# Kernel tuning notes

Hardware: AMD Instinct MI355X
Metric: run time of the kernel (lower is better)

Reference implementation:

```python
import jax, jax.numpy as jnp
import numpy as np

S, B, D, H, E, HID = 512, 16, 768, 12, 8, 3072
HD = D // H
EPS = 1e-5


def _ln(x, w, b):
    m = jnp.mean(x, axis=-1, keepdims=True)
    v = jnp.var(x, axis=-1, keepdims=True)
    return (x - m) * jax.lax.rsqrt(v + EPS) * w + b


def setup_inputs() -> dict:
    key = jax.random.key(0)
    ks = jax.random.split(key, 9)
    n = lambda k, *sh: jax.random.normal(k, sh, dtype=jnp.float32) * 0.02
    return dict(
        x=jax.random.normal(ks[0], (S, B, D), dtype=jnp.float32),
        ln1_w=jnp.ones((D,), jnp.float32), ln1_b=jnp.zeros((D,), jnp.float32),
        wq=n(ks[1], D, D), bq=jnp.zeros((D,), jnp.float32),
        wk=n(ks[2], D, D), bk=jnp.zeros((D,), jnp.float32),
        wv=n(ks[3], D, D), bv=jnp.zeros((D,), jnp.float32),
        wo=n(ks[4], D, D), bo=jnp.zeros((D,), jnp.float32),
        ln2_w=jnp.ones((D,), jnp.float32), ln2_b=jnp.zeros((D,), jnp.float32),
        wg=n(ks[5], D, E), bg=jnp.zeros((E,), jnp.float32),
        w1=n(ks[6], E, D, HID), b1=jnp.zeros((E, HID), jnp.float32),
        w2=n(ks[7], E, HID, D), b2=jnp.zeros((E, D), jnp.float32),
    )


def _block(x, ln1_w, ln1_b, wq, bq, wk, bk, wv, bv, wo, bo,
           ln2_w, ln2_b, wg, bg, w1, b1, w2, b2):
    # --- attention: source uses query = norm1(x), key = value = x ---
    q_in = _ln(x, ln1_w, ln1_b)
    q = (q_in @ wq + bq).reshape(S, B, H, HD)
    k = (x @ wk + bk).reshape(S, B, H, HD)
    v = (x @ wv + bv).reshape(S, B, H, HD)
    scores = jnp.einsum('sbhd,tbhd->bhst', q, k) * (1.0 / HD ** 0.5)
    p = jax.nn.softmax(scores, axis=-1)
    attn = jnp.einsum('bhst,tbhd->sbhd', p, v).reshape(S, B, D)
    x = x + attn @ wo + bo
    # --- top-1 MoE MLP on norm2(x) ---
    t = _ln(x, ln2_w, ln2_b).reshape(S * B, D)   # [T, D] routed tokens
    logits = t @ wg + bg                          # [T, E]
    probs = jax.nn.softmax(logits, axis=-1)
    idx = jnp.argmax(logits, axis=-1)             # top-1 expert per token
    gate = jnp.take_along_axis(probs, idx[:, None], axis=-1)   # [T, 1]
    comb = jax.nn.one_hot(idx, E, dtype=t.dtype) * gate        # [T, E]

    def expert(w1e, b1e, w2e, b2e):
        return jax.nn.gelu(t @ w1e + b1e, approximate=False) @ w2e + b2e

    y = jax.vmap(expert)(w1, b1, w2, b2)          # [E, T, D]
    moe = jnp.einsum('te,etd->td', comb, y).reshape(S, B, D)
    return x + moe


def reference(x, ln1_w, ln1_b, wq, bq, wk, bk, wv, bv, wo, bo,
              ln2_w, ln2_b, wg, bg, w1, b1, w2, b2):
    return _block(x, ln1_w, ln1_b, wq, bq, wk, bk, wv, bv, wo, bo,
                  ln2_w, ln2_b, wg, bg, w1, b1, w2, b2)
```

## Files before the change

kernel.cpp:

```cpp
#include <hip/hip_runtime.h>
#include <math.h>

#define SS 512
#define BB 16
#define DD 768
#define HH 12
#define HDIM 64
#define EE 8
#define HID 3072
#define TT 8192
#define EPSV 1e-5f
#define KVSTR 1536
#define ASTR 72
#define NBANK 64

typedef __attribute__((ext_vector_type(8))) short s16x8;
typedef __attribute__((ext_vector_type(4))) short s16x4;
typedef __attribute__((ext_vector_type(4))) float f32x4;

__device__ inline short f2bf(float f) {
  unsigned u = __builtin_bit_cast(unsigned, f);
  unsigned r = (u + 0x7fffu + ((u >> 16) & 1u)) >> 16;
  return (short)r;
}

__device__ inline float gelu_f(float x) {
  float y = 0.7978845608028654f * (x + 0.044715f * x * x * x);
  float e = __expf(2.f * y);
  float t = 1.f - 2.f / (e + 1.f);
  return 0.5f * x * (1.f + t);
}

__device__ inline void gl2lds16(const void* g, void* l) {
  __builtin_amdgcn_global_load_lds(
      (const __attribute__((address_space(1))) unsigned int*)g,
      (__attribute__((address_space(3))) unsigned int*)l, 16, 0, 0);
}

__global__ __launch_bounds__(256) void transpose4_bf16(const float* __restrict__ w0,
    const float* __restrict__ w1p, const float* __restrict__ w2p,
    const float* __restrict__ w3p, short* __restrict__ dst) {
  const int z = blockIdx.z;
  const float* W = (z == 0) ? w0 : (z == 1) ? w1p : (z == 2) ? w2p : w3p;
  short* Wt = dst + (size_t)z * DD * DD;
  int k0 = blockIdx.x * 64, n0 = blockIdx.y * 64;
  __shared__ float t[64][65];
  for (int i = threadIdx.x; i < 1024; i += 256) {
    int r = i >> 4, c4 = (i & 15) << 2;
    const float4 v = *(const float4*)(W + (size_t)(k0 + r) * DD + n0 + c4);
    t[r][c4] = v.x; t[r][c4 + 1] = v.y; t[r][c4 + 2] = v.z; t[r][c4 + 3] = v.w;
  }
  __syncthreads();
  for (int i = threadIdx.x; i < 1024; i += 256) {
    int r = i >> 4, c4 = (i & 15) << 2;
    s16x4 sv;
    sv.x = f2bf(t[c4][r]);     sv.y = f2bf(t[c4 + 1][r]);
    sv.z = f2bf(t[c4 + 2][r]); sv.w = f2bf(t[c4 + 3][r]);
    *(s16x4*)(Wt + (size_t)(n0 + r) * DD + k0 + c4) = sv;
  }
}

__global__ __launch_bounds__(256) void transpose_bf16(const float* __restrict__ W,
    short* __restrict__ Wt, int K, int N) {
  const float* Wz = W + (size_t)blockIdx.z * K * N;
  short* Wtz = Wt + (size_t)blockIdx.z * K * N;
  int k0 = blockIdx.x * 64, n0 = blockIdx.y * 64;
  __shared__ float t[64][65];
  for (int i = threadIdx.x; i < 1024; i += 256) {
    int r = i >> 4, c4 = (i & 15) << 2;
    const float4 v = *(const float4*)(Wz + (size_t)(k0 + r) * N + n0 + c4);
    t[r][c4] = v.x; t[r][c4 + 1] = v.y; t[r][c4 + 2] = v.z; t[r][c4 + 3] = v.w;
  }
  __syncthreads();
  for (int i = threadIdx.x; i < 1024; i += 256) {
    int r = i >> 4, c4 = (i & 15) << 2;
    s16x4 sv;
    sv.x = f2bf(t[c4][r]);     sv.y = f2bf(t[c4 + 1][r]);
    sv.z = f2bf(t[c4 + 2][r]); sv.w = f2bf(t[c4 + 3][r]);
    *(s16x4*)(Wtz + (size_t)(n0 + r) * K + k0 + c4) = sv;
  }
}

__global__ __launch_bounds__(256) void gate_transpose(const float* __restrict__ wg,
    float* __restrict__ wgT) {
  for (int i = threadIdx.x + blockIdx.x * 256; i < EE * DD; i += 256 * 8) {
    int e = i / DD, d = i - e * DD;
    wgT[i] = wg[d * EE + e];
  }
}

__global__ __launch_bounds__(256) void fused_cvt_ln1(const float* __restrict__ x,
    const float* __restrict__ w, const float* __restrict__ b,
    short* __restrict__ xbf, short* __restrict__ ln1bf) {
  const int tok = blockIdx.x * 4 + (threadIdx.x >> 6);
  const int lane = threadIdx.x & 63;
  const float* row = x + (size_t)tok * DD;
  const float4 v0 = *(const float4*)(row + lane * 4);
  const float4 v1 = *(const float4*)(row + 256 + lane * 4);
  const float4 v2 = *(const float4*)(row + 512 + lane * 4);
  float s = v0.x + v0.y + v0.z + v0.w + v1.x + v1.y + v1.z + v1.w
          + v2.x + v2.y + v2.z + v2.w;
  float ss = v0.x * v0.x + v0.y * v0.y + v0.z * v0.z + v0.w * v0.w
           + v1.x * v1.x + v1.y * v1.y + v1.z * v1.z + v1.w * v1.w
           + v2.x * v2.x + v2.y * v2.y + v2.z * v2.z + v2.w * v2.w;
#pragma unroll
  for (int o = 1; o < 64; o <<= 1) { s += __shfl_xor(s, o); ss += __shfl_xor(ss, o); }
  const float mean = s * (1.f / DD);
  const float inv = rsqrtf(ss * (1.f / DD) - mean * mean + EPSV);
  short* xrow = xbf + (size_t)tok * DD;
  short* lrow = ln1bf + (size_t)tok * DD;
#define LN1_CHUNK(v, off) { \
  const float4 wv = *(const float4*)(w + (off) + lane * 4); \
  const float4 bv = *(const float4*)(b + (off) + lane * 4); \
  s16x4 xa, la; \
  xa.x = f2bf(v.x); xa.y = f2bf(v.y); xa.z = f2bf(v.z); xa.w = f2bf(v.w); \
  la.x = f2bf((v.x - mean) * inv * wv.x + bv.x); \
  la.y = f2bf((v.y - mean) * inv * wv.y + bv.y); \
  la.z = f2bf((v.z - mean) * inv * wv.z + bv.z); \
  la.w = f2bf((v.w - mean) * inv * wv.w + bv.w); \
  *(s16x4*)(xrow + (off) + lane * 4) = xa; \
  *(s16x4*)(lrow + (off) + lane * 4) = la; }
  LN1_CHUNK(v0, 0)
  LN1_CHUNK(v1, 256)
  LN1_CHUNK(v2, 512)
#undef LN1_CHUNK
}

__global__ __launch_bounds__(256) void fused_ln2_route(const float* __restrict__ x1,
    const float* __restrict__ w, const float* __restrict__ b,
    const float* __restrict__ wgT, const float* __restrict__ bg,
    short* __restrict__ tlnbf, int* __restrict__ idx, float* __restrict__ gate,
    int* __restrict__ cnt2) {
  const int tok = blockIdx.x * 4 + (threadIdx.x >> 6);
  const int lane = threadIdx.x & 63;
  const float* row = x1 + (size_t)tok * DD;
  const float4 v0 = *(const float4*)(row + lane * 4);
  const float4 v1 = *(const float4*)(row + 256 + lane * 4);
  const float4 v2 = *(const float4*)(row + 512 + lane * 4);
  float s = v0.x + v0.y + v0.z + v0.w + v1.x + v1.y + v1.z + v1.w
          + v2.x + v2.y + v2.z + v2.w;
  float ss = v0.x * v0.x + v0.y * v0.y + v0.z * v0.z + v0.w * v0.w
           + v1.x * v1.x + v1.y * v1.y + v1.z * v1.z + v1.w * v1.w
           + v2.x * v2.x + v2.y * v2.y + v2.z * v2.z + v2.w * v2.w;
#pragma unroll
  for (int o = 1; o < 64; o <<= 1) { s += __shfl_xor(s, o); ss += __shfl_xor(ss, o); }
  const float mean = s * (1.f / DD);
  const float inv = rsqrtf(ss * (1.f / DD) - mean * mean + EPSV);
  short* srow = tlnbf + (size_t)tok * DD;
  float acc[EE];
#pragma unroll
  for (int e = 0; e < EE; ++e) acc[e] = 0.f;
#define LN2_CHUNK(v, off) { \
  const float4 wv = *(const float4*)(w + (off) + lane * 4); \
  const float4 bv = *(const float4*)(b + (off) + lane * 4); \
  float4 n; \
  n.x = (v.x - mean) * inv * wv.x + bv.x; \
  n.y = (v.y - mean) * inv * wv.y + bv.y; \
  n.z = (v.z - mean) * inv * wv.z + bv.z; \
  n.w = (v.w - mean) * inv * wv.w + bv.w; \
  s16x4 sv; sv.x = f2bf(n.x); sv.y = f2bf(n.y); sv.z = f2bf(n.z); sv.w = f2bf(n.w); \
  *(s16x4*)(srow + (off) + lane * 4) = sv; \
  const int i0 = (off) + lane * 4; \
  _Pragma("unroll") \
  for (int e = 0; e < EE; ++e) { \
    const float4 g = *(const float4*)(wgT + (size_t)e * DD + i0); \
    acc[e] += n.x * g.x + n.y * g.y + n.z * g.z + n.w * g.w; } }
  LN2_CHUNK(v0, 0)
  LN2_CHUNK(v1, 256)
  LN2_CHUNK(v2, 512)
#undef LN2_CHUNK
#pragma unroll
  for (int o = 1; o < 64; o <<= 1)
#pragma unroll
    for (int e = 0; e < EE; ++e) acc[e] += __shfl_xor(acc[e], o);
  if (lane == 0) {
#pragma unroll
    for (int e = 0; e < EE; ++e) acc[e] += bg[e];
    int best = 0; float bm = acc[0];
#pragma unroll
    for (int e = 1; e < EE; ++e) if (acc[e] > bm) { bm = acc[e]; best = e; }
    float sum = 0.f;
#pragma unroll
    for (int e = 0; e < EE; ++e) sum += __expf(acc[e] - bm);
    idx[tok] = best;
    gate[tok] = 1.0f / sum;
    atomicAdd(&cnt2[(blockIdx.x & (NBANK - 1)) * 16 + best], 1);
  }
}

__global__ void prefix2_kernel(const int* __restrict__ cnt2, int* __restrict__ cnt,
                               int* __restrict__ off, int* __restrict__ tb,
                               int* __restrict__ bankbase) {
  const int lane = threadIdx.x;
  int c[EE], excl[EE], tot[EE];
#pragma unroll
  for (int e = 0; e < EE; ++e) c[e] = cnt2[lane * 16 + e];
#pragma unroll
  for (int e = 0; e < EE; ++e) {
    int x = c[e];
#pragma unroll
    for (int o = 1; o < 64; o <<= 1) {
      int y = __shfl_up(x, o);
      if (lane >= o) x += y;
    }
    excl[e] = x - c[e];
    tot[e] = __shfl(x, 63);
  }
  int oo = 0;
  int offl[EE];
#pragma unroll
  for (int e = 0; e < EE; ++e) { offl[e] = oo; oo += tot[e]; }
#pragma unroll
  for (int e = 0; e < EE; ++e)
    bankbase[lane * EE + e] = offl[e] + excl[e];
  if (lane == 0) {
    int o = 0, t = 0;
    for (int e = 0; e < EE; ++e) {
      off[e] = o; tb[e] = t; cnt[e] = tot[e];
      o += tot[e]; t += (tot[e] + 127) >> 7;
    }
    off[EE] = o; tb[EE] = t;
  }
}

__global__ __launch_bounds__(256) void scatter_kernel(const int* __restrict__ idx,
    const int* __restrict__ bankbase, int* __restrict__ cur2, int* __restrict__ perm) {
  int t = blockIdx.x * 256 + threadIdx.x;
  if (t < TT) {
    int e = idx[t];
    int bank = (t >> 2) & (NBANK - 1);
    int p = atomicAdd(&cur2[bank * 16 + e], 1);
    perm[bankbase[bank * EE + e] + p] = t;
  }
}

template<int MODE, int OUTBF, int COLS>
__global__ __launch_bounds__(256) void mgemm(const short* __restrict__ A,
    const short* __restrict__ Wt, const float* __restrict__ bias,
    const float* __restrict__ bias2, const float* __restrict__ res,
    void* __restrict__ C, int N, int K) {
  const int bx = blockIdx.x;
  const int lid = bx >> 3;
  const int colt = lid >> 3, rband = lid & 7;
  const int bm = (((bx & 7) << 3) + rband) * 128;
  const int bn = colt * COLS;
  constexpr int NJ = COLS / 32;
  __shared__ short As[128 * 32];
  __shared__ short Bs[COLS * 32];
  const int tid = threadIdx.x;
  const int wave = tid >> 6, lane = tid & 63;
  const int wr = (wave >> 1) * 64, wc = (wave & 1) * (COLS / 2);
  const int l16 = lane & 15, quad = lane >> 4;
  const int kq = (((lane & 3) ^ ((lane >> 3) & 3)) << 3);
  const int sw = ((l16 >> 1) & 3);
  const short* Ab = A + (size_t)(bm + (wave << 5) + (lane >> 2)) * K + kq;
  const short* Bb = Wt + (size_t)(bn + wave * (COLS / 4) + (lane >> 2)) * K + kq;
  short* lA = &As[(wave << 5) * 32];
  short* lB = &Bs[wave * (COLS / 4) * 32];
  f32x4 acc[4][NJ] = {};
  for (int k0 = 0; k0 < K; k0 += 32) {
    gl2lds16(Ab + k0, lA);
    gl2lds16(Ab + (size_t)16 * K + k0, lA + 512);
    gl2lds16(Bb + k0, lB);
    if (COLS == 128) gl2lds16(Bb + (size_t)16 * K + k0, lB + 512);
    __syncthreads();
    s16x8 af[4], bfr[NJ];
#pragma unroll
    for (int i = 0; i < 4; ++i)
      af[i] = *(s16x8*)(&As[(wr + i * 16 + l16) * 32 + ((quad ^ sw) << 3)]);
#pragma unroll
    for (int j = 0; j < NJ; ++j)
      bfr[j] = *(s16x8*)(&Bs[(wc + j * 16 + l16) * 32 + ((quad ^ sw) << 3)]);
#pragma unroll
    for (int i = 0; i < 4; ++i)
#pragma unroll
      for (int j = 0; j < NJ; ++j)
        acc[i][j] = __builtin_amdgcn_mfma_f32_16x16x32_bf16(af[i], bfr[j], acc[i][j], 0, 0, 0);
    __syncthreads();
  }
#pragma unroll
  for (int i = 0; i < 4; ++i) {
#pragma unroll
    for (int r = 0; r < 4; ++r) {
      int row = bm + wr + i * 16 + quad * 4 + r;
#pragma unroll
      for (int j = 0; j < NJ; ++j) {
        int col = bn + wc + j * 16 + l16;
        float bv = (MODE == 2) ? (col >= DD ? bias2[col - DD] : bias[col]) : bias[col];
        float val = acc[i][j][r] + bv;
        if (MODE == 1) val += res[(size_t)row * N + col];
        if (OUTBF) ((short*)C)[(size_t)row * N + col] = f2bf(val);
        else       ((float*)C)[(size_t)row * N + col] = val;
      }
    }
  }
}

__global__ __launch_bounds__(256) void qkv_mgemm(const short* __restrict__ ln1bf,
    const short* __restrict__ xbf, const short* __restrict__ wqT,
    const short* __restrict__ kvT, const float* __restrict__ bq,
    const float* __restrict__ bk, const float* __restrict__ bv,
    short* __restrict__ qbf, short* __restrict__ kvbf) {
  const int bx = blockIdx.x;
  const int lid = bx >> 3;
  const int colt = lid >> 3, rband = lid & 7;
  const int bm = (((bx & 7) << 3) + rband) * 128;
  const bool isQ = (colt < 6);
  const int bn = isQ ? colt * 128 : (colt - 6) * 128;
  const short* A  = isQ ? ln1bf : xbf;
  const short* Bt = isQ ? wqT : kvT;
  const float* bias = isQ ? bq : (bn < DD ? bk : bv);
  const int bofs = (!isQ && bn >= DD) ? DD : 0;
  short* out = isQ ? qbf : kvbf;
  const int OS = isQ ? DD : KVSTR;
  const int K = DD;
  __shared__ short As[128 * 32];
  __shared__ short Bs[128 * 32];
  const int tid = threadIdx.x;
  const int wave = tid >> 6, lane = tid & 63;
  const int wr = (wave >> 1) * 64, wc = (wave & 1) * 64;
  const int l16 = lane & 15, quad = lane >> 4;
  const int kq = (((lane & 3) ^ ((lane >> 3) & 3)) << 3);
  const int sw = ((l16 >> 1) & 3);
  const short* Ab = A + (size_t)(bm + (wave << 5) + (lane >> 2)) * K + kq;
  const short* Bb = Bt + (size_t)(bn + (wave << 5) + (lane >> 2)) * K + kq;
  short* lA = &As[(wave << 5) * 32];
  short* lB = &Bs[(wave << 5) * 32];
  f32x4 acc[4][4] = {};
  for (int k0 = 0; k0 < K; k0 += 32) {
    gl2lds16(Ab + k0, lA);
    gl2lds16(Ab + (size_t)16 * K + k0, lA + 512);
    gl2lds16(Bb + k0, lB);
    gl2lds16(Bb + (size_t)16 * K + k0, lB + 512);
    __syncthreads();
    s16x8 af[4], bfr[4];
#pragma unroll
    for (int i = 0; i < 4; ++i)
      af[i] = *(s16x8*)(&As[(wr + i * 16 + l16) * 32 + ((quad ^ sw) << 3)]);
#pragma unroll
    for (int j = 0; j < 4; ++j)
      bfr[j] = *(s16x8*)(&Bs[(wc + j * 16 + l16) * 32 + ((quad ^ sw) << 3)]);
#pragma unroll
    for (int i = 0; i < 4; ++i)
#pragma unroll
      for (int j = 0; j < 4; ++j)
        acc[i][j] = __builtin_amdgcn_mfma_f32_16x16x32_bf16(af[i], bfr[j], acc[i][j], 0, 0, 0);
    __syncthreads();
  }
#pragma unroll
  for (int i = 0; i < 4; ++i) {
#pragma unroll
    for (int r = 0; r < 4; ++r) {
      int row = bm + wr + i * 16 + quad * 4 + r;
#pragma unroll
      for (int j = 0; j < 4; ++j) {
        int col = bn + wc + j * 16 + l16;
        float val = acc[i][j][r] + bias[col - bofs];
        out[(size_t)row * OS + col] = f2bf(val);
      }
    }
  }
}

__global__ __launch_bounds__(256) void attn_mfma(const short* __restrict__ q,
    const short* __restrict__ k, const short* __restrict__ v, short* __restrict__ o) {
  const int qt = blockIdx.x, bidx = blockIdx.y, hidx = blockIdx.z;
  const int tid = threadIdx.x;
  const int wave = tid >> 6, lane = tid & 63;
  const int l16 = lane & 15, quad = lane >> 4;
  const int s0 = qt * 64;
  __shared__ short Qs[64 * ASTR];
  __shared__ short Ks[64 * ASTR];
  __shared__ short Vs[64 * ASTR];
  __shared__ short Ps[64 * ASTR];
  for (int i = tid; i < 512; i += 256) {
    int r = i >> 3, c8 = i & 7;
    *(s16x8*)(&Qs[r * ASTR + c8 * 8]) =
        *(const s16x8*)(q + ((size_t)(s0 + r) * BB + bidx) * DD + hidx * HDIM + c8 * 8);
  }
  __syncthreads();
  s16x8 af0 = *(s16x8*)(&Qs[(wave * 16 + l16) * ASTR + quad * 8]);
  s16x8 af1 = *(s16x8*)(&Qs[(wave * 16 + l16) * ASTR + 32 + quad * 8]);
  f32x4 oacc[4] = {};
  float mr[4], lr[4];
#pragma unroll
  for (int r = 0; r < 4; ++r) { mr[r] = -1e30f; lr[r] = 0.f; }

  for (int t0 = 0; t0 < SS; t0 += 64) {
    __syncthreads();
    for (int i = tid; i < 512; i += 256) {
      int r = i >> 3, c8 = i & 7;
      *(s16x8*)(&Ks[r * ASTR + c8 * 8]) =
          *(const s16x8*)(k + ((size_t)(t0 + r) * BB + bidx) * KVSTR + hidx * HDIM + c8 * 8);
    }
    for (int i = tid; i < 1024; i += 256) {
      int r = i >> 4, c4 = i & 15;
      s16x4 vv = *(const s16x4*)(v + ((size_t)(t0 + r) * BB + bidx) * KVSTR + hidx * HDIM + c4 * 4);
      Vs[(c4 * 4 + 0) * ASTR + r] = vv.x;
      Vs[(c4 * 4 + 1) * ASTR + r] = vv.y;
      Vs[(c4 * 4 + 2) * ASTR + r] = vv.z;
      Vs[(c4 * 4 + 3) * ASTR + r] = vv.w;
    }
    __syncthreads();
    f32x4 sc[4];
    const f32x4 zero = {};
#pragma unroll
    for (int j = 0; j < 4; ++j) {
      s16x8 kf0 = *(s16x8*)(&Ks[(j * 16 + l16) * ASTR + quad * 8]);
      s16x8 kf1 = *(s16x8*)(&Ks[(j * 16 + l16) * ASTR + 32 + quad * 8]);
      sc[j] = __builtin_amdgcn_mfma_f32_16x16x32_bf16(af0, kf0, zero, 0, 0, 0);
      sc[j] = __builtin_amdgcn_mfma_f32_16x16x32_bf16(af1, kf1, sc[j], 0, 0, 0);
#pragma unroll
      for (int r = 0; r < 4; ++r) sc[j][r] *= 0.125f;
    }
    float tm[4], alpha[4], rs[4];
#pragma unroll
    for (int r = 0; r < 4; ++r) {
      tm[r] = mr[r];
#pragma unroll
      for (int j = 0; j < 4; ++j) tm[r] = fmaxf(tm[r], sc[j][r]);
    }
#pragma unroll
    for (int mask = 1; mask < 16; mask <<= 1)
#pragma unroll
      for (int r = 0; r < 4; ++r) tm[r] = fmaxf(tm[r], __shfl_xor(tm[r], mask));
#pragma unroll
    for (int r = 0; r < 4; ++r) { alpha[r] = __expf(mr[r] - tm[r]); mr[r] = tm[r]; rs[r] = 0.f; }
#pragma unroll
    for (int j = 0; j < 4; ++j)
#pragma unroll
      for (int r = 0; r < 4; ++r) {
        float p = __expf(sc[j][r] - tm[r]);
        sc[j][r] = p; rs[r] += p;
      }
#pragma unroll
    for (int mask = 1; mask < 16; mask <<= 1)
#pragma unroll
      for (int r = 0; r < 4; ++r) rs[r] += __shfl_xor(rs[r], mask);
#pragma unroll
    for (int r = 0; r < 4; ++r) lr[r] = lr[r] * alpha[r] + rs[r];
#pragma unroll
    for (int j = 0; j < 4; ++j)
#pragma unroll
      for (int r = 0; r < 4; ++r)
        Ps[(wave * 16 + quad * 4 + r) * ASTR + j * 16 + l16] = f2bf(sc[j][r]);
#pragma unroll
    for (int jd = 0; jd < 4; ++jd)
#pragma unroll
      for (int r = 0; r < 4; ++r) oacc[jd][r] *= alpha[r];
    __syncthreads();
    s16x8 pf0 = *(s16x8*)(&Ps[(wave * 16 + l16) * ASTR + quad * 8]);
    s16x8 pf1 = *(s16x8*)(&Ps[(wave * 16 + l16) * ASTR + 32 + quad * 8]);
#pragma unroll
    for (int jd = 0; jd < 4; ++jd) {
      s16x8 vf0 = *(s16x8*)(&Vs[(jd * 16 + l16) * ASTR + quad * 8]);
      s16x8 vf1 = *(s16x8*)(&Vs[(jd * 16 + l16) * ASTR + 32 + quad * 8]);
      oacc[jd] = __builtin_amdgcn_mfma_f32_16x16x32_bf16(pf0, vf0, oacc[jd], 0, 0, 0);
      oacc[jd] = __builtin_amdgcn_mfma_f32_16x16x32_bf16(pf1, vf1, oacc[jd], 0, 0, 0);
    }
  }
#pragma unroll
  for (int r = 0; r < 4; ++r) {
    int row = s0 + wave * 16 + quad * 4 + r;
    float invl = 1.f / lr[r];
#pragma unroll
    for (int jd = 0; jd < 4; ++jd) {
      int d = jd * 16 + l16;
      o[((size_t)row * BB + bidx) * DD + hidx * HDIM + d] = f2bf(oacc[jd][r] * invl);
    }
  }
}

__global__ __launch_bounds__(256) void egemm1(const short* __restrict__ tlnbf,
    const short* __restrict__ w1t, const float* __restrict__ b1,
    const int* __restrict__ off, const int* __restrict__ tb, const int* __restrict__ cnt,
    const int* __restrict__ perm, short* __restrict__ hbuf) {
  const int bx = blockIdx.x;
  const int lid = bx >> 3;
  const int rband = lid % 9, colt = lid / 9;
  const int row = (bx & 7) * 9 + rband;
  if (row >= tb[EE]) return;
  int e = 0;
  while (e < EE - 1 && tb[e + 1] <= row) ++e;
  const int lt = row - tb[e];
  const int cnte = cnt[e];
  const int slot0 = off[e] + lt * 128;
  const int slast = off[e] + cnte - 1;
  const int bn = colt * 128;
  const int tid = threadIdx.x;
  const int wave = tid >> 6, lane = tid & 63;
  const int wr = (wave >> 1) * 64, wc = (wave & 1) * 64;
  const int l16 = lane & 15, quad = lane >> 4;
  const int kq = (((lane & 3) ^ ((lane >> 3) & 3)) << 3);
  const int sw = ((l16 >> 1) & 3);
  __shared__ short As[128 * 32];
  __shared__ short Bs[128 * 32];
  f32x4 acc[4][4] = {};
  const int sA = slot0 + (wave << 5) + (lane >> 2);
  const int tokA = perm[sA <= slast ? sA : slast];
  const int tokB = perm[(sA + 16) <= slast ? (sA + 16) : slast];
  const short* AbA = tlnbf + (size_t)tokA * DD + kq;
  const short* AbB = tlnbf + (size_t)tokB * DD + kq;
  const short* Bb = w1t + (size_t)e * DD * HID
                  + (size_t)(bn + (wave << 5) + (lane >> 2)) * DD + kq;
  short* lA = &As[(wave << 5) * 32];
  short* lB = &Bs[(wave << 5) * 32];
  for (int k0 = 0; k0 < DD; k0 += 32) {
    gl2lds16(AbA + k0, lA);
    gl2lds16(AbB + k0, lA + 512);
    gl2lds16(Bb + k0, lB);
    gl2lds16(Bb + (size_t)16 * DD + k0, lB + 512);
    __syncthreads();
    s16x8 af[4], bfr[4];
#pragma unroll
    for (int i = 0; i < 4; ++i)
      af[i] = *(s16x8*)(&As[(wr + i * 16 + l16) * 32 + ((quad ^ sw) << 3)]);
#pragma unroll
    for (int j = 0; j < 4; ++j)
      bfr[j] = *(s16x8*)(&Bs[(wc + j * 16 + l16) * 32 + ((quad ^ sw) << 3)]);
#pragma unroll
    for (int i = 0; i < 4; ++i)
#pragma unroll
      for (int j = 0; j < 4; ++j)
        acc[i][j] = __builtin_amdgcn_mfma_f32_16x16x32_bf16(af[i], bfr[j], acc[i][j], 0, 0, 0);
    __syncthreads();
  }
#pragma unroll
  for (int i = 0; i < 4; ++i) {
#pragma unroll
    for (int r = 0; r < 4; ++r) {
      int rl = wr + i * 16 + quad * 4 + r;
      if (lt * 128 + rl >= cnte) continue;
#pragma unroll
      for (int j = 0; j < 4; ++j) {
        int col = bn + wc + j * 16 + l16;
        float xv = acc[i][j][r] + b1[e * HID + col];
        hbuf[(size_t)(slot0 + rl) * HID + col] = f2bf(gelu_f(xv));
      }
    }
  }
}

__global__ __launch_bounds__(256) void egemm2(const short* __restrict__ hbuf,
    const short* __restrict__ w2t, const float* __restrict__ b2,
    const int* __restrict__ perm, const int* __restrict__ off,
    const int* __restrict__ tb, const int* __restrict__ cnt,
    const float* __restrict__ gate, const float* __restrict__ x1,
    float* __restrict__ out) {
  const int bx = blockIdx.x;
  const int lid = bx >> 3;
  const int colt = lid % 12, rband = lid / 12;
  const int row = (bx & 7) * 9 + rband;
  if (row >= tb[EE]) return;
  int e = 0;
  while (e < EE - 1 && tb[e + 1] <= row) ++e;
  const int lt = row - tb[e];
  const int cnte = cnt[e];
  const int slot0 = off[e] + lt * 128;
  const int bn = colt * 64;
  const int tid = threadIdx.x;
  const int wave = tid >> 6, lane = tid & 63;
  const int wr = (wave >> 1) * 64, wc = (wave & 1) * 32;
  const int l16 = lane & 15, quad = lane >> 4;
  const int kq = (((lane & 3) ^ ((lane >> 3) & 3)) << 3);
  const int sw = ((l16 >> 1) & 3);
  __shared__ short As[128 * 32];
  __shared__ short Bs[64 * 32];
  __shared__ int stok[128];
  if (tid < 128) stok[tid] = (lt * 128 + tid < cnte) ? perm[slot0 + tid] : -1;
  f32x4 acc[4][2] = {};
  const short* Ab = hbuf + (size_t)(slot0 + (wave << 5) + (lane >> 2)) * HID + kq;
  const short* Bb = w2t + (size_t)e * HID * DD
                  + (size_t)(bn + wave * 16 + (lane >> 2)) * HID + kq;
  short* lA = &As[(wave << 5) * 32];
  short* lB = &Bs[wave * 16 * 32];
  for (int k0 = 0; k0 < HID; k0 += 32) {
    gl2lds16(Ab + k0, lA);
    gl2lds16(Ab + (size_t)16 * HID + k0, lA + 512);
    gl2lds16(Bb + k0, lB);
    __syncthreads();
    s16x8 af[4], bfr[2];
#pragma unroll
    for (int i = 0; i < 4; ++i)
      af[i] = *(s16x8*)(&As[(wr + i * 16 + l16) * 32 + ((quad ^ sw) << 3)]);
#pragma unroll
    for (int j = 0; j < 2; ++j)
      bfr[j] = *(s16x8*)(&Bs[(wc + j * 16 + l16) * 32 + ((quad ^ sw) << 3)]);
#pragma unroll
    for (int i = 0; i < 4; ++i)
#pragma unroll
      for (int j = 0; j < 2; ++j)
        acc[i][j] = __builtin_amdgcn_mfma_f32_16x16x32_bf16(af[i], bfr[j], acc[i][j], 0, 0, 0);
    __syncthreads();
  }
#pragma unroll
  for (int i = 0; i < 4; ++i) {
#pragma unroll
    for (int r = 0; r < 4; ++r) {
      int rl = wr + i * 16 + quad * 4 + r;
      if (lt * 128 + rl >= cnte) continue;
      int tok = stok[rl];
      float g = gate[tok];
#pragma unroll
      for (int j = 0; j < 2; ++j) {
        int col = bn + wc + j * 16 + l16;
        float val = acc[i][j][r] + b2[e * DD + col];
        out[(size_t)tok * DD + col] = x1[(size_t)tok * DD + col] + g * val;
      }
    }
  }
}

extern "C" void kernel_launch(void* const* d_in, const int* in_sizes, int n_in,
                              void* d_out, int out_size, void* d_ws, size_t ws_size,
                              hipStream_t stream) {
  const float* x     = (const float*)d_in[0];
  const float* ln1_w = (const float*)d_in[1];
  const float* ln1_b = (const float*)d_in[2];
  const float* wq    = (const float*)d_in[3];
  const float* bq    = (const float*)d_in[4];
  const float* wk    = (const float*)d_in[5];
  const float* bk    = (const float*)d_in[6];
  const float* wv    = (const float*)d_in[7];
  const float* bv    = (const float*)d_in[8];
  const float* wo    = (const float*)d_in[9];
  const float* bo    = (const float*)d_in[10];
  const float* ln2_w = (const float*)d_in[11];
  const float* ln2_b = (const float*)d_in[12];
  const float* wg    = (const float*)d_in[13];
  const float* bg    = (const float*)d_in[14];
  const float* w1    = (const float*)d_in[15];
  const float* b1    = (const float*)d_in[16];
  const float* w2    = (const float*)d_in[17];
  const float* b2    = (const float*)d_in[18];
  float* out = (float*)d_out;
  float* ws = (float*)d_ws;

  const size_t TD = (size_t)TT * DD;
  float* x1    = ws;
  short* tlnbf = (short*)(ws + TD);
  short* sbase = (short*)(ws + 2 * TD);
  short* xbf   = sbase;
  short* ln1bf = sbase + TD + 128 * DD;
  short* attbf = ln1bf;
  short* qbf   = ln1bf + TD;
  short* kvbf  = qbf + TD;
  short* hbuf  = kvbf + (size_t)TT * KVSTR;
  short* wqT   = hbuf + (size_t)(TT + 128) * HID;
  short* kvT   = wqT + (size_t)DD * DD;
  short* woT   = kvT + (size_t)KVSTR * DD;
  short* w1T   = woT + (size_t)DD * DD;
  short* w2T   = w1T + (size_t)EE * DD * HID;
  int*   meta  = (int*)(w2T + (size_t)EE * HID * DD);
  int*   idx   = meta;
  float* gate  = (float*)(meta + TT);
  int*   perm  = meta + 2 * TT;
  int*   cnt2  = meta + 3 * TT;
  int*   cur2  = cnt2 + NBANK * 16;
  int*   bankbase = cur2 + NBANK * 16;
  int*   cnt   = bankbase + NBANK * EE;
  int*   off   = cnt + 8;
  int*   tb    = off + 9;
  float* wgT   = (float*)(tb + 9);

  hipMemsetAsync(cnt2, 0, 2 * NBANK * 16 * sizeof(int), stream);

  transpose4_bf16<<<dim3(12, 12, 4), 256, 0, stream>>>(wq, wk, wv, wo, wqT);
  transpose_bf16<<<dim3(12, 48, 8), 256, 0, stream>>>(w1, w1T, DD, HID);
  transpose_bf16<<<dim3(48, 12, 8), 256, 0, stream>>>(w2, w2T, HID, DD);
  gate_transpose<<<8, 256, 0, stream>>>(wg, wgT);

  fused_cvt_ln1<<<TT / 4, 256, 0, stream>>>(x, ln1_w, ln1_b, xbf, ln1bf);

  qkv_mgemm<<<8 * 8 * 18, 256, 0, stream>>>(ln1bf, xbf, wqT, kvT, bq, bk, bv, qbf, kvbf);

  attn_mfma<<<dim3(SS / 64, BB, HH), 256, 0, stream>>>(qbf, kvbf, kvbf + DD, attbf);

  mgemm<1, 0, 64><<<64 * 12, 256, 0, stream>>>(attbf, woT, bo, nullptr, x, x1, DD, DD);

  fused_ln2_route<<<TT / 4, 256, 0, stream>>>(x1, ln2_w, ln2_b, wgT, bg,
                                              tlnbf, idx, gate, cnt2);
  prefix2_kernel<<<1, 64, 0, stream>>>(cnt2, cnt, off, tb, bankbase);
  scatter_kernel<<<TT / 256, 256, 0, stream>>>(idx, bankbase, cur2, perm);

  egemm1<<<8 * 9 * 24, 256, 0, stream>>>(tlnbf, w1T, b1, off, tb, cnt, perm, hbuf);
  egemm2<<<8 * 9 * 12, 256, 0, stream>>>(hbuf, w2T, b2, perm, off, tb, cnt, gate, x1, out);
}
```

Before: 575.0 us.

## Double-buffer LDS staging in expert GEMMs and widen egemm2 K-tile

Both expert GEMM kernels now use two LDS buffers, prefetching the next K slice with async global-to-LDS loads while MFMAs run on the current slice. Synchronisation uses explicit vmcnt/lgkmcnt waits and raw barriers instead of two __syncthreads per step. egemm2 also doubles its K tile to 64 with a wider 8-way XOR swizzle, halving loop iterations and barriers. The cost is more LDS per block, which may reduce occupancy, and hand-tuned waitcnt values that must match the number of in-flight loads.

```diff
diff --git a/kernel.cpp b/kernel.cpp
--- a/kernel.cpp
+++ b/kernel.cpp
@@ -493,8 +493,8 @@
   const int l16 = lane & 15, quad = lane >> 4;
   const int kq = (((lane & 3) ^ ((lane >> 3) & 3)) << 3);
   const int sw = ((l16 >> 1) & 3);
-  __shared__ short As[128 * 32];
-  __shared__ short Bs[128 * 32];
+  __shared__ short As[2][128 * 32];
+  __shared__ short Bs[2][128 * 32];
   f32x4 acc[4][4] = {};
   const int sA = slot0 + (wave << 5) + (lane >> 2);
   const int tokA = perm[sA <= slast ? sA : slast];
@@ -503,28 +503,36 @@
   const short* AbB = tlnbf + (size_t)tokB * DD + kq;
   const short* Bb = w1t + (size_t)e * DD * HID
                   + (size_t)(bn + (wave << 5) + (lane >> 2)) * DD + kq;
-  short* lA = &As[(wave << 5) * 32];
-  short* lB = &Bs[(wave << 5) * 32];
-  for (int k0 = 0; k0 < DD; k0 += 32) {
-    gl2lds16(AbA + k0, lA);
-    gl2lds16(AbB + k0, lA + 512);
-    gl2lds16(Bb + k0, lB);
-    gl2lds16(Bb + (size_t)16 * DD + k0, lB + 512);
-    __syncthreads();
+  const int lofs = (wave << 5) * 32;
+#define STAGE_E1(p, k0) { \
+  gl2lds16(AbA + (k0), &As[p][lofs]); \
+  gl2lds16(AbB + (k0), &As[p][lofs + 512]); \
+  gl2lds16(Bb + (k0), &Bs[p][lofs]); \
+  gl2lds16(Bb + (size_t)16 * DD + (k0), &Bs[p][lofs + 512]); }
+  STAGE_E1(0, 0)
+  int p = 0;
+  for (int t = 0; t < 24; ++t) {
+    const int kn = (t + 1 < 24 ? t + 1 : 23) * 32;
+    STAGE_E1(p ^ 1, kn)
+    asm volatile("s_waitcnt vmcnt(4)" ::: "memory");
+    __builtin_amdgcn_s_barrier();
     s16x8 af[4], bfr[4];
 #pragma unroll
     for (int i = 0; i < 4; ++i)
-      af[i] = *(s16x8*)(&As[(wr + i * 16 + l16) * 32 + ((quad ^ sw) << 3)]);
+      af[i] = *(s16x8*)(&As[p][(wr + i * 16 + l16) * 32 + ((quad ^ sw) << 3)]);
 #pragma unroll
     for (int j = 0; j < 4; ++j)
-      bfr[j] = *(s16x8*)(&Bs[(wc + j * 16 + l16) * 32 + ((quad ^ sw) << 3)]);
+      bfr[j] = *(s16x8*)(&Bs[p][(wc + j * 16 + l16) * 32 + ((quad ^ sw) << 3)]);
 #pragma unroll
     for (int i = 0; i < 4; ++i)
 #pragma unroll
       for (int j = 0; j < 4; ++j)
         acc[i][j] = __builtin_amdgcn_mfma_f32_16x16x32_bf16(af[i], bfr[j], acc[i][j], 0, 0, 0);
-    __syncthreads();
-  }
+    asm volatile("s_waitcnt lgkmcnt(0)" ::: "memory");
+    __builtin_amdgcn_s_barrier();
+    p ^= 1;
+  }
+#undef STAGE_E1
 #pragma unroll
   for (int i = 0; i < 4; ++i) {
 #pragma unroll
@@ -562,37 +570,53 @@
   const int wave = tid >> 6, lane = tid & 63;
   const int wr = (wave >> 1) * 64, wc = (wave & 1) * 32;
   const int l16 = lane & 15, quad = lane >> 4;
-  const int kq = (((lane & 3) ^ ((lane >> 3) & 3)) << 3);
-  const int sw = ((l16 >> 1) & 3);
-  __shared__ short As[128 * 32];
-  __shared__ short Bs[64 * 32];
+  const int rg = lane >> 3;
+  const int kq8 = (((lane & 7) ^ rg) << 3);
+  const int swz = l16 & 7;
+  __shared__ short As[2][128 * 64];
+  __shared__ short Bs[2][64 * 64];
   __shared__ int stok[128];
   if (tid < 128) stok[tid] = (lt * 128 + tid < cnte) ? perm[slot0 + tid] : -1;
   f32x4 acc[4][2] = {};
-  const short* Ab = hbuf + (size_t)(slot0 + (wave << 5) + (lane >> 2)) * HID + kq;
+  const short* Ab = hbuf + (size_t)(slot0 + (wave << 5) + rg) * HID + kq8;
   const short* Bb = w2t + (size_t)e * HID * DD
-                  + (size_t)(bn + wave * 16 + (lane >> 2)) * HID + kq;
-  short* lA = &As[(wave << 5) * 32];
-  short* lB = &Bs[wave * 16 * 32];
-  for (int k0 = 0; k0 < HID; k0 += 32) {
-    gl2lds16(Ab + k0, lA);
-    gl2lds16(Ab + (size_t)16 * HID + k0, lA + 512);
-    gl2lds16(Bb + k0, lB);
-    __syncthreads();
-    s16x8 af[4], bfr[2];
-#pragma unroll
-    for (int i = 0; i < 4; ++i)
-      af[i] = *(s16x8*)(&As[(wr + i * 16 + l16) * 32 + ((quad ^ sw) << 3)]);
-#pragma unroll
-    for (int j = 0; j < 2; ++j)
-      bfr[j] = *(s16x8*)(&Bs[(wc + j * 16 + l16) * 32 + ((quad ^ sw) << 3)]);
-#pragma unroll
-    for (int i = 0; i < 4; ++i)
+                  + (size_t)(bn + wave * 16 + rg) * HID + kq8;
+  const int lofsA = (wave << 5) * 64;
+  const int lofsB = wave * 16 * 64;
+#define STAGE_E2(p, k0) { \
+  gl2lds16(Ab + (k0), &As[p][lofsA]); \
+  gl2lds16(Ab + (size_t)8 * HID + (k0), &As[p][lofsA + 512]); \
+  gl2lds16(Ab + (size_t)16 * HID + (k0), &As[p][lofsA + 1024]); \
+  gl2lds16(Ab + (size_t)24 * HID + (k0), &As[p][lofsA + 1536]); \
+  gl2lds16(Bb + (k0), &Bs[p][lofsB]); \
+  gl2lds16(Bb + (size_t)8 * HID + (k0), &Bs[p][lofsB + 512]); }
+  STAGE_E2(0, 0)
+  int p = 0;
+  for (int t = 0; t < 48; ++t) {
+    const int kn = (t + 1 < 48 ? t + 1 : 47) * 64;
+    STAGE_E2(p ^ 1, kn)
+    asm volatile("s_waitcnt vmcnt(6)" ::: "memory");
+    __builtin_amdgcn_s_barrier();
+#pragma unroll
+    for (int h = 0; h < 2; ++h) {
+      s16x8 af[4], bfr[2];
+#pragma unroll
+      for (int i = 0; i < 4; ++i)
+        af[i] = *(s16x8*)(&As[p][(wr + i * 16 + l16) * 64 + (((quad + 4 * h) ^ swz) << 3)]);
 #pragma unroll
       for (int j = 0; j < 2; ++j)
-        acc[i][j] = __builtin_amdgcn_mfma_f32_16x16x32_bf16(af[i], bfr[j], acc[i][j], 0, 0, 0);
-    __syncthreads();
-  }
+        bfr[j] = *(s16x8*)(&Bs[p][(wc + j * 16 + l16) * 64 + (((quad + 4 * h) ^ swz) << 3)]);
+#pragma unroll
+      for (int i = 0; i < 4; ++i)
+#pragma unroll
+        for (int j = 0; j < 2; ++j)
+          acc[i][j] = __builtin_amdgcn_mfma_f32_16x16x32_bf16(af[i], bfr[j], acc[i][j], 0, 0, 0);
+    }
+    asm volatile("s_waitcnt lgkmcnt(0)" ::: "memory");
+    __builtin_amdgcn_s_barrier();
+    p ^= 1;
+  }
+#undef STAGE_E2
 #pragma unroll
   for (int i = 0; i < 4; ++i) {
 #pragma unroll
```

New measurement: 599.9 us. +4.3%, slower.
